# Optimization experiments

Measured on AMD Instinct MI355X. Metric: run time of the kernel, lower is better.

The kernel has to match this reference:

```python
import jax, jax.numpy as jnp
import numpy as np

B, T, D = 1, 4096, 2048
H, G, K = 16, 4, 128   # query heads, kv heads, head_dim
R = H // G             # n_rep = 4
EPS = 1e-6
SCALE = K ** -0.5


def rms_norm(x, scale):
    var = jnp.mean(x.astype(jnp.float32) ** 2, axis=-1, keepdims=True)
    normed = x * jax.lax.rsqrt(var + EPS)
    return (scale * normed).astype(x.dtype)


def apply_rope(x_BTHK, sin_BTK, cos_BTK):
    half = x_BTHK.shape[-1] // 2
    x1, x2 = x_BTHK[..., :half], x_BTHK[..., half:]
    s = sin_BTK[:, :, None, :]
    c = cos_BTK[:, :, None, :]
    return jnp.concatenate([x1 * c - x2 * s, x2 * c + x1 * s], axis=-1).astype(x_BTHK.dtype)


def setup_inputs() -> dict:
    key = jax.random.key(0)
    ks = jax.random.split(key, 8)
    hidden = jax.random.normal(ks[0], (B, T, D), dtype=jnp.float32)
    # rope angles
    inv_freq = 1.0 / (10000.0 ** (jnp.arange(0, K, 2, dtype=jnp.float32) / K))  # [K/2]
    pos = jnp.arange(T, dtype=jnp.float32)
    ang = pos[:, None] * inv_freq[None, :]          # [T, K/2]
    sin = jnp.broadcast_to(jnp.sin(ang)[None], (B, T, K // 2))
    cos = jnp.broadcast_to(jnp.cos(ang)[None], (B, T, K // 2))
    mask = jnp.broadcast_to(jnp.tril(jnp.ones((T, T), dtype=bool))[None], (B, T, T))
    std = D ** -0.5
    Wq = jax.random.normal(ks[1], (D, H * K), dtype=jnp.float32) * std
    Wk = jax.random.normal(ks[2], (D, G * K), dtype=jnp.float32) * std
    Wv = jax.random.normal(ks[3], (D, G * K), dtype=jnp.float32) * std
    Wo = jax.random.normal(ks[4], (H * K, D), dtype=jnp.float32) * ((H * K) ** -0.5)
    q_scale = jnp.ones((K,), dtype=jnp.float32)
    k_scale = jnp.ones((K,), dtype=jnp.float32)
    return {"hidden_BTD": hidden, "sin_BTK": sin, "cos_BTK": cos, "mask": mask,
            "Wq": Wq, "Wk": Wk, "Wv": Wv, "Wo": Wo,
            "q_scale": q_scale, "k_scale": k_scale}


def reference(hidden_BTD, sin_BTK, cos_BTK, mask, Wq, Wk, Wv, Wo, q_scale, k_scale):
    q = rms_norm((hidden_BTD @ Wq).reshape(B, T, H, K), q_scale)
    k = rms_norm((hidden_BTD @ Wk).reshape(B, T, G, K), k_scale)
    v = (hidden_BTD @ Wv).reshape(B, T, G, K)
    q = apply_rope(q, sin_BTK, cos_BTK)
    k = apply_rope(k, sin_BTK, cos_BTK)
    q_BTGRK = q.reshape(B, T, G, R, K)
    logits = jnp.einsum('BTGRK,BSGK->BTSGR', q_BTGRK, k) * SCALE
    neg = float(jnp.finfo(logits.dtype).min)
    logits = jnp.where(mask[:, :, :, None, None], logits, neg)
    weights = jax.nn.softmax(logits.astype(jnp.float32), axis=2).astype(logits.dtype)
    attn = jnp.einsum('BTSGR,BSGK->BTGRK', weights, v)
    return attn.reshape(B, T, H * K) @ Wo
```

## Files before the change

### kernel.cpp

```cpp
#include <hip/hip_runtime.h>
#include <hip/hip_bf16.h>
#include <stdint.h>

#define T_SEQ 4096
#define KVB 64
#define BM 128
#define BN 128
#define BK 64
#define SCL2 (0.08838834764831845f * 1.44269504088896340f)

typedef unsigned short u16;
typedef __attribute__((ext_vector_type(8))) short s16x8;
typedef __attribute__((ext_vector_type(4))) short s16x4;
typedef __attribute__((ext_vector_type(4))) float f32x4;

__device__ __forceinline__ u16 f2bf(float f) {
  union { float f; unsigned u; } a; a.f = f;
  unsigned r = a.u + 0x7fffu + ((a.u >> 16) & 1u);
  return (u16)(r >> 16);
}
__device__ __forceinline__ float bf2f(u16 b) {
  union { unsigned u; float f; } a; a.u = ((unsigned)b) << 16;
  return a.f;
}
__device__ __forceinline__ unsigned cvtpk(float lo, float hi) {
  unsigned r;
  asm volatile("v_cvt_pk_bf16_f32 %0, %1, %2" : "=v"(r) : "v"(lo), "v"(hi));
  return r;
}

__device__ __forceinline__ void gl_lds16(const void* g, void* l) {
  __builtin_amdgcn_global_load_lds((const __attribute__((address_space(1))) void*)g,
                                   (__attribute__((address_space(3))) void*)l, 16, 0, 0);
}

__global__ __launch_bounds__(256) void k_cvt(const float* __restrict__ in, u16* __restrict__ out) {
  int i = (blockIdx.x * 256 + threadIdx.x) * 8;
  const float4* p = (const float4*)(in + i);
  float4 a = p[0], b = p[1];
  s16x8 o;
  o[0] = (short)f2bf(a.x); o[1] = (short)f2bf(a.y); o[2] = (short)f2bf(a.z); o[3] = (short)f2bf(a.w);
  o[4] = (short)f2bf(b.x); o[5] = (short)f2bf(b.y); o[6] = (short)f2bf(b.z); o[7] = (short)f2bf(b.w);
  *(s16x8*)(out + i) = o;
}

__global__ __launch_bounds__(256) void k_transpose_cvt(const float* __restrict__ in, u16* __restrict__ out,
                                                       int R, int C) {
  __shared__ float tile[32][33];
  int c0 = blockIdx.x * 32, r0 = blockIdx.y * 32;
  int tx = threadIdx.x & 31, ty = threadIdx.x >> 5;
#pragma unroll
  for (int k = 0; k < 4; k++) tile[ty + 8 * k][tx] = in[(size_t)(r0 + ty + 8 * k) * C + c0 + tx];
  __syncthreads();
#pragma unroll
  for (int k = 0; k < 4; k++) out[(size_t)(c0 + ty + 8 * k) * R + r0 + tx] = f2bf(tile[tx][ty + 8 * k]);
}

__global__ __launch_bounds__(256, 2) void k_gemm(const u16* __restrict__ A, const u16* __restrict__ Bt,
                                                 u16* __restrict__ Cq, u16* __restrict__ Ck, u16* __restrict__ Cvt,
                                                 float* __restrict__ Cf, int M, int N, int Kd, int mode) {
  __shared__ u16 SM[BM * BK + BN * BK];
  u16* As = SM;
  u16* Bs = SM + BM * BK;
  int tid = threadIdx.x, lane = tid & 63, w = tid >> 6;
  int g = lane >> 4, r16 = lane & 15;
  int m0 = blockIdx.y * BM, n0 = blockIdx.x * BN;
  int wr = w >> 1, wc = w & 1;
  f32x4 acc[4][4] = {};

  for (int kt = 0; kt < Kd; kt += BK) {
#pragma unroll
    for (int i = 0; i < 4; i++) {
      int idx = i * 256 + tid;
      int row = idx >> 3, c = idx & 7;
      int cs = c ^ (row & 7);
      gl_lds16(A + (size_t)(m0 + row) * Kd + kt + cs * 8, As + (i * 256 + w * 64) * 8);
    }
#pragma unroll
    for (int i = 0; i < 4; i++) {
      int idx = i * 256 + tid;
      int row = idx >> 3, c = idx & 7;
      int cs = c ^ (row & 7);
      gl_lds16(Bt + (size_t)(n0 + row) * Kd + kt + cs * 8, Bs + (i * 256 + w * 64) * 8);
    }
    __syncthreads();
#pragma unroll
    for (int kk = 0; kk < 2; kk++) {
      s16x8 af[4], bfr[4];
#pragma unroll
      for (int mi = 0; mi < 4; mi++) {
        int row = wr * 64 + mi * 16 + r16;
        af[mi] = *(const s16x8*)(As + row * 64 + (((kk * 4 + g) ^ (row & 7)) * 8));
      }
#pragma unroll
      for (int ni = 0; ni < 4; ni++) {
        int row = wc * 64 + ni * 16 + r16;
        bfr[ni] = *(const s16x8*)(Bs + row * 64 + (((kk * 4 + g) ^ (row & 7)) * 8));
      }
#pragma unroll
      for (int mi = 0; mi < 4; mi++)
#pragma unroll
        for (int ni = 0; ni < 4; ni++)
          acc[mi][ni] = __builtin_amdgcn_mfma_f32_16x16x32_bf16(af[mi], bfr[ni], acc[mi][ni], 0, 0, 0);
    }
    __syncthreads();
  }

#pragma unroll
  for (int mi = 0; mi < 4; mi++) {
    int rowb = m0 + wr * 64 + mi * 16 + g * 4;
#pragma unroll
    for (int ni = 0; ni < 4; ni++) {
      int ncol0 = n0 + wc * 64 + ni * 16;
      int col = ncol0 + r16;
      if (mode == 0) {
        if (ncol0 < 2048) {
#pragma unroll
          for (int j = 0; j < 4; j++) Cq[(size_t)(rowb + j) * 2048 + col] = f2bf(acc[mi][ni][j]);
        } else if (ncol0 < 2560) {
#pragma unroll
          for (int j = 0; j < 4; j++) Ck[(size_t)(rowb + j) * 512 + (col - 2048)] = f2bf(acc[mi][ni][j]);
        } else {
          s16x4 pk;
#pragma unroll
          for (int j = 0; j < 4; j++) pk[j] = (short)f2bf(acc[mi][ni][j]);
          *(s16x4*)(Cvt + (size_t)(col - 2560) * T_SEQ + rowb) = pk;
        }
      } else {
#pragma unroll
        for (int j = 0; j < 4; j++) Cf[(size_t)(rowb + j) * N + col] = acc[mi][ni][j];
      }
    }
  }
}

__global__ __launch_bounds__(256) void k_normrope(u16* __restrict__ Q, u16* __restrict__ Kc,
                                                  const float* __restrict__ sinT, const float* __restrict__ cosT,
                                                  const float* __restrict__ qsc, const float* __restrict__ ksc) {
  int t = blockIdx.x;
  int w = threadIdx.x >> 6, lane = threadIdx.x & 63;
  int unit = blockIdx.y * 4 + w;
  u16* base;
  const float* sc;
  float fold;
  if (unit < 16) { base = Q + (size_t)t * 2048 + unit * 128; sc = qsc; fold = SCL2; }
  else { base = Kc + (size_t)t * 512 + (unit - 16) * 128; sc = ksc; fold = 1.0f; }
  float x1 = bf2f(base[lane]), x2 = bf2f(base[lane + 64]);
  float ss = x1 * x1 + x2 * x2;
#pragma unroll
  for (int off = 32; off >= 1; off >>= 1) ss += __shfl_xor(ss, off);
  float rinv = rsqrtf(ss * (1.0f / 128.0f) + 1e-6f);
  float n1 = x1 * rinv * sc[lane], n2 = x2 * rinv * sc[lane + 64];
  float s = sinT[t * 64 + lane], c = cosT[t * 64 + lane];
  base[lane] = f2bf((n1 * c - n2 * s) * fold);
  base[lane + 64] = f2bf((n2 * c + n1 * s) * fold);
}

__global__ __launch_bounds__(256, 2) void k_attn(const u16* __restrict__ Q, const u16* __restrict__ Kc,
                                                 const u16* __restrict__ Vt, u16* __restrict__ O) {
  __shared__ u16 SM[36864];
  int tid = threadIdx.x, lane = tid & 63, w = tid >> 6;
  int g = lane >> 4, r16 = lane & 15;

  int bid = blockIdx.x;
  int xcd = bid & 7;
  int k = bid >> 3;
  int slot = k >> 5;
  int c = k & 31;
  int h = xcd * 2 + (c & 1);
  int qb = slot ? (31 - (c >> 1)) : (c >> 1);
  int gh = h >> 2;
  int q0 = qb * 128, qw = q0 + w * 32;
  int nt = 2 * qb + 2;

  s16x8 qf[2][4];
#pragma unroll
  for (int qc = 0; qc < 2; qc++)
#pragma unroll
    for (int dc = 0; dc < 4; dc++)
      qf[qc][dc] = *(const s16x8*)(Q + (size_t)(qw + qc * 16 + r16) * 2048 + h * 128 + dc * 32 + g * 8);

  auto STAGE = [&](int bb, int tt) {
    int kv0 = tt * KVB;
    u16* Kb = SM + bb * 8192;
    u16* Vb = SM + 16384 + bb * 8192;
#pragma unroll
    for (int i = 0; i < 4; i++) {
      int idx = i * 256 + tid;
      int row = idx >> 4, cc = idx & 15;
      int cs = cc ^ (row & 7);
      gl_lds16(Kc + (size_t)(kv0 + row) * 512 + gh * 128 + cs * 8, Kb + (i * 256 + w * 64) * 8);
    }
#pragma unroll
    for (int i = 0; i < 4; i++) {
      int idx = i * 256 + tid;
      int row = idx >> 3, cc = idx & 7;
      int cs = cc ^ (row & 7);
      gl_lds16(Vt + (size_t)(gh * 128 + row) * T_SEQ + kv0 + cs * 8, Vb + (i * 256 + w * 64) * 8);
    }
  };

  f32x4 acc[2][8] = {};
  float mrun[2] = {-3.0e38f, -3.0e38f};
  float lrun[2] = {0.0f, 0.0f};

  STAGE(0, 0);
  __syncthreads();

  for (int t = 0; t < nt; ++t) {
    int kv0 = t * KVB;
    int bb = t & 1;
    STAGE(bb ^ 1, (t + 1 < nt) ? t + 1 : 0);

    if (kv0 <= qw + 31) {
      u16* Kb = SM + bb * 8192;
      u16* Vb = SM + 16384 + bb * 8192;
      u16* Pw = SM + 32768 + w * 1024;

      f32x4 sv[2][4] = {};
      __builtin_amdgcn_s_setprio(1);
#pragma unroll
      for (int kc = 0; kc < 4; kc++) {
        int krow = kc * 16 + r16;
#pragma unroll
        for (int dc = 0; dc < 4; dc++) {
          s16x8 kf = *(const s16x8*)(Kb + krow * 128 + (((dc * 4 + g) ^ (krow & 7)) * 8));
          sv[0][kc] = __builtin_amdgcn_mfma_f32_16x16x32_bf16(kf, qf[0][dc], sv[0][kc], 0, 0, 0);
          sv[1][kc] = __builtin_amdgcn_mfma_f32_16x16x32_bf16(kf, qf[1][dc], sv[1][kc], 0, 0, 0);
        }
      }
      __builtin_amdgcn_s_setprio(0);

#pragma unroll
      for (int qc = 0; qc < 2; qc++) {
        int qg = qw + qc * 16 + r16;
        bool needmask = (kv0 + KVB - 1) > (qw + qc * 16);
        if (needmask) {
#pragma unroll
          for (int kc = 0; kc < 4; kc++)
#pragma unroll
            for (int j2 = 0; j2 < 4; j2++)
              if (kv0 + kc * 16 + g * 4 + j2 > qg) sv[qc][kc][j2] = -3.0e38f;
        }
        float mt = sv[qc][0][0];
#pragma unroll
        for (int kc = 0; kc < 4; kc++)
#pragma unroll
          for (int j2 = 0; j2 < 4; j2++) mt = fmaxf(mt, sv[qc][kc][j2]);
        mt = fmaxf(mt, __shfl_xor(mt, 16));
        mt = fmaxf(mt, __shfl_xor(mt, 32));
        if (__any(mt > mrun[qc] + 8.0f)) {
          float mnew = fmaxf(mrun[qc], mt);
          float al = exp2f(mrun[qc] - mnew);
          mrun[qc] = mnew;
          lrun[qc] *= al;
#pragma unroll
          for (int df = 0; df < 8; df++) acc[qc][df] = acc[qc][df] * al;
        }
        float rs = 0.0f;
#pragma unroll
        for (int kc = 0; kc < 4; kc++) {
          float p0 = exp2f(sv[qc][kc][0] - mrun[qc]);
          float p1 = exp2f(sv[qc][kc][1] - mrun[qc]);
          float p2 = exp2f(sv[qc][kc][2] - mrun[qc]);
          float p3 = exp2f(sv[qc][kc][3] - mrun[qc]);
          rs += (p0 + p1) + (p2 + p3);
          uint2 pk;
          pk.x = cvtpk(p0, p1);
          pk.y = cvtpk(p2, p3);
          int pslot = (kc * 2 + (g >> 1)) ^ (r16 & 7);
          *(uint2*)((char*)Pw + r16 * 128 + pslot * 16 + (g & 1) * 8) = pk;
        }
        rs += __shfl_xor(rs, 16);
        rs += __shfl_xor(rs, 32);
        lrun[qc] += rs;

        __builtin_amdgcn_s_setprio(1);
#pragma unroll
        for (int st = 0; st < 2; st++) {
          s16x8 pf = *(const s16x8*)((char*)Pw + r16 * 128 + (((st * 4 + g) ^ (r16 & 7)) * 16));
#pragma unroll
          for (int df = 0; df < 8; df++) {
            int vrow = df * 16 + r16;
            s16x8 vf = *(const s16x8*)(Vb + vrow * 64 + (((st * 4 + g) ^ (vrow & 7)) * 8));
            acc[qc][df] = __builtin_amdgcn_mfma_f32_16x16x32_bf16(vf, pf, acc[qc][df], 0, 0, 0);
          }
        }
        __builtin_amdgcn_s_setprio(0);
      }
    }
    __syncthreads();
  }

  char* ob = (char*)SM + w * 8192;
#pragma unroll
  for (int qc = 0; qc < 2; qc++) {
    float linv = 1.0f / lrun[qc];
#pragma unroll
    for (int df = 0; df < 8; df++) {
      s16x4 pk;
#pragma unroll
      for (int j2 = 0; j2 < 4; j2++) pk[j2] = (short)f2bf(acc[qc][df][j2] * linv);
      int row = qc * 16 + r16;
      int c16 = df * 2 + (g >> 1);
      *(s16x4*)(ob + row * 256 + ((c16 ^ (row & 7)) << 4) + (g & 1) * 8) = pk;
    }
  }
#pragma unroll
  for (int i = 0; i < 8; i++) {
    int idx = i * 64 + lane;
    int row = idx >> 4, cc = idx & 15;
    s16x8 v = *(const s16x8*)(ob + row * 256 + ((cc ^ (row & 7)) << 4));
    *(s16x8*)(O + (size_t)(qw + row) * 2048 + h * 128 + cc * 8) = v;
  }
}

extern "C" void kernel_launch(void* const* d_in, const int* in_sizes, int n_in,
                              void* d_out, int out_size, void* d_ws, size_t ws_size,
                              hipStream_t stream) {
  const float* hidden = (const float*)d_in[0];
  const float* sinT = (const float*)d_in[1];
  const float* cosT = (const float*)d_in[2];
  const float* Wq = (const float*)d_in[4];
  const float* Wk = (const float*)d_in[5];
  const float* Wv = (const float*)d_in[6];
  const float* Wo = (const float*)d_in[7];
  const float* qsc = (const float*)d_in[8];
  const float* ksc = (const float*)d_in[9];
  float* out = (float*)d_out;

  char* ws = (char*)d_ws;
  u16* Xb   = (u16*)(ws + 0);
  u16* Bqkv = (u16*)(ws + 16777216);
  u16* Wot  = (u16*)(ws + 29360128);
  u16* Qraw = (u16*)(ws + 37748736);
  u16* Kraw = (u16*)(ws + 54525952);
  u16* Vt   = (u16*)(ws + 58720256);
  u16* Oat  = (u16*)(ws + 62914560);

  k_cvt<<<dim3(4096), dim3(256), 0, stream>>>(hidden, Xb);
  k_transpose_cvt<<<dim3(64, 64), dim3(256), 0, stream>>>(Wq, Bqkv, 2048, 2048);
  k_transpose_cvt<<<dim3(16, 64), dim3(256), 0, stream>>>(Wk, Bqkv + 2048 * 2048, 2048, 512);
  k_transpose_cvt<<<dim3(16, 64), dim3(256), 0, stream>>>(Wv, Bqkv + 2560 * 2048, 2048, 512);
  k_transpose_cvt<<<dim3(64, 64), dim3(256), 0, stream>>>(Wo, Wot, 2048, 2048);

  k_gemm<<<dim3(24, 32), dim3(256), 0, stream>>>(Xb, Bqkv, Qraw, Kraw, Vt, (float*)nullptr,
                                                 4096, 3072, 2048, 0);
  k_normrope<<<dim3(4096, 5), dim3(256), 0, stream>>>(Qraw, Kraw, sinT, cosT, qsc, ksc);
  k_attn<<<dim3(512), dim3(256), 0, stream>>>(Qraw, Kraw, Vt, Oat);
  k_gemm<<<dim3(16, 32), dim3(256), 0, stream>>>(Oat, Wot, (u16*)nullptr, (u16*)nullptr, (u16*)nullptr,
                                                 out, 4096, 2048, 2048, 1);
}
```

Measured before the change: 274.4 us.

## Split attention KV tiles across wave pairs with smaller query blocks and LDS merge

The attention kernel now uses 64-row query blocks, 1024 blocks in total, ordered longest-first. The four waves form two query halves by two KV halves, so each wave handles 32 queries against 32 of the 64 staged KV rows. The partial softmax states (max, sum, accumulator) of the two KV-split waves are merged through LDS at the end before the bf16 write. This aims to raise parallelism and improve causal load balance, at the cost of more LDS (72KB, which may limit occupancy) and an extra reduction pass.

```diff
diff --git a/kernel.cpp b/kernel.cpp
--- a/kernel.cpp
+++ b/kernel.cpp
@@ -158,32 +158,32 @@
 
 __global__ __launch_bounds__(256, 2) void k_attn(const u16* __restrict__ Q, const u16* __restrict__ Kc,
                                                  const u16* __restrict__ Vt, u16* __restrict__ O) {
-  __shared__ u16 SM[36864];
+  __shared__ __align__(16) char SMc[73728];
   int tid = threadIdx.x, lane = tid & 63, w = tid >> 6;
   int g = lane >> 4, r16 = lane & 15;
+  int qs = w >> 1, ks = w & 1;
 
   int bid = blockIdx.x;
   int xcd = bid & 7;
-  int k = bid >> 3;
-  int slot = k >> 5;
-  int c = k & 31;
-  int h = xcd * 2 + (c & 1);
-  int qb = slot ? (31 - (c >> 1)) : (c >> 1);
+  int lid = bid >> 3;
+  int h = xcd * 2 + (lid & 1);
+  int qb = 63 - (lid >> 1);
   int gh = h >> 2;
-  int q0 = qb * 128, qw = q0 + w * 32;
-  int nt = 2 * qb + 2;
+  int q0 = qb * 64;
+  int qwv = q0 + qs * 32;
+  int nt = qb + 1;
 
   s16x8 qf[2][4];
 #pragma unroll
   for (int qc = 0; qc < 2; qc++)
 #pragma unroll
     for (int dc = 0; dc < 4; dc++)
-      qf[qc][dc] = *(const s16x8*)(Q + (size_t)(qw + qc * 16 + r16) * 2048 + h * 128 + dc * 32 + g * 8);
+      qf[qc][dc] = *(const s16x8*)(Q + (size_t)(qwv + qc * 16 + r16) * 2048 + h * 128 + dc * 32 + g * 8);
 
   auto STAGE = [&](int bb, int tt) {
     int kv0 = tt * KVB;
-    u16* Kb = SM + bb * 8192;
-    u16* Vb = SM + 16384 + bb * 8192;
+    u16* Kb = (u16*)(SMc + bb * 16384);
+    u16* Vb = (u16*)(SMc + 32768 + bb * 16384);
 #pragma unroll
     for (int i = 0; i < 4; i++) {
       int idx = i * 256 + tid;
@@ -212,19 +212,20 @@
     int bb = t & 1;
     STAGE(bb ^ 1, (t + 1 < nt) ? t + 1 : 0);
 
-    if (kv0 <= qw + 31) {
-      u16* Kb = SM + bb * 8192;
-      u16* Vb = SM + 16384 + bb * 8192;
-      u16* Pw = SM + 32768 + w * 1024;
-
-      f32x4 sv[2][4] = {};
+    int kvw = kv0 + ks * 32;
+    if (kvw <= qwv + 31) {
+      u16* Kb = (u16*)(SMc + bb * 16384);
+      u16* Vb = (u16*)(SMc + 32768 + bb * 16384);
+      char* Pwb = SMc + 65536 + w * 2048;
+
+      f32x4 sv[2][2] = {};
       __builtin_amdgcn_s_setprio(1);
 #pragma unroll
-      for (int kc = 0; kc < 4; kc++) {
-        int krow = kc * 16 + r16;
+      for (int kc = 0; kc < 2; kc++) {
+        int krow = ks * 32 + kc * 16 + r16;
 #pragma unroll
         for (int dc = 0; dc < 4; dc++) {
-          s16x8 kf = *(const s16x8*)(Kb + krow * 128 + (((dc * 4 + g) ^ (krow & 7)) * 8));
+          s16x8 kf = *(const s16x8*)((u16*)Kb + krow * 128 + (((dc * 4 + g) ^ (krow & 7)) * 8));
           sv[0][kc] = __builtin_amdgcn_mfma_f32_16x16x32_bf16(kf, qf[0][dc], sv[0][kc], 0, 0, 0);
           sv[1][kc] = __builtin_amdgcn_mfma_f32_16x16x32_bf16(kf, qf[1][dc], sv[1][kc], 0, 0, 0);
         }
@@ -233,18 +234,18 @@
 
 #pragma unroll
       for (int qc = 0; qc < 2; qc++) {
-        int qg = qw + qc * 16 + r16;
-        bool needmask = (kv0 + KVB - 1) > (qw + qc * 16);
+        int qg = qwv + qc * 16 + r16;
+        bool needmask = (kvw + 31) > (qwv + qc * 16);
         if (needmask) {
 #pragma unroll
-          for (int kc = 0; kc < 4; kc++)
+          for (int kc = 0; kc < 2; kc++)
 #pragma unroll
             for (int j2 = 0; j2 < 4; j2++)
-              if (kv0 + kc * 16 + g * 4 + j2 > qg) sv[qc][kc][j2] = -3.0e38f;
+              if (kvw + kc * 16 + g * 4 + j2 > qg) sv[qc][kc][j2] = -3.0e38f;
         }
         float mt = sv[qc][0][0];
 #pragma unroll
-        for (int kc = 0; kc < 4; kc++)
+        for (int kc = 0; kc < 2; kc++)
 #pragma unroll
           for (int j2 = 0; j2 < 4; j2++) mt = fmaxf(mt, sv[qc][kc][j2]);
         mt = fmaxf(mt, __shfl_xor(mt, 16));
@@ -259,7 +260,7 @@
         }
         float rs = 0.0f;
 #pragma unroll
-        for (int kc = 0; kc < 4; kc++) {
+        for (int kc = 0; kc < 2; kc++) {
           float p0 = exp2f(sv[qc][kc][0] - mrun[qc]);
           float p1 = exp2f(sv[qc][kc][1] - mrun[qc]);
           float p2 = exp2f(sv[qc][kc][2] - mrun[qc]);
@@ -268,50 +269,75 @@
           uint2 pk;
           pk.x = cvtpk(p0, p1);
           pk.y = cvtpk(p2, p3);
-          int pslot = (kc * 2 + (g >> 1)) ^ (r16 & 7);
-          *(uint2*)((char*)Pw + r16 * 128 + pslot * 16 + (g & 1) * 8) = pk;
+          int unit = ((qc << 2) | (kc << 1) | (g >> 1)) ^ (r16 & 7);
+          *(uint2*)(Pwb + r16 * 128 + unit * 16 + (g & 1) * 8) = pk;
         }
         rs += __shfl_xor(rs, 16);
         rs += __shfl_xor(rs, 32);
         lrun[qc] += rs;
-
-        __builtin_amdgcn_s_setprio(1);
-#pragma unroll
-        for (int st = 0; st < 2; st++) {
-          s16x8 pf = *(const s16x8*)((char*)Pw + r16 * 128 + (((st * 4 + g) ^ (r16 & 7)) * 16));
-#pragma unroll
-          for (int df = 0; df < 8; df++) {
-            int vrow = df * 16 + r16;
-            s16x8 vf = *(const s16x8*)(Vb + vrow * 64 + (((st * 4 + g) ^ (vrow & 7)) * 8));
-            acc[qc][df] = __builtin_amdgcn_mfma_f32_16x16x32_bf16(vf, pf, acc[qc][df], 0, 0, 0);
-          }
-        }
-        __builtin_amdgcn_s_setprio(0);
-      }
+      }
+
+      __builtin_amdgcn_s_setprio(1);
+      s16x8 pf0 = *(const s16x8*)(Pwb + r16 * 128 + (((0 * 4 + g) ^ (r16 & 7)) * 16));
+      s16x8 pf1 = *(const s16x8*)(Pwb + r16 * 128 + (((1 * 4 + g) ^ (r16 & 7)) * 16));
+#pragma unroll
+      for (int df = 0; df < 8; df++) {
+        int vrow = df * 16 + r16;
+        s16x8 vf = *(const s16x8*)((u16*)Vb + vrow * 64 + (((ks * 4 + g) ^ (vrow & 7)) * 8));
+        acc[0][df] = __builtin_amdgcn_mfma_f32_16x16x32_bf16(vf, pf0, acc[0][df], 0, 0, 0);
+        acc[1][df] = __builtin_amdgcn_mfma_f32_16x16x32_bf16(vf, pf1, acc[1][df], 0, 0, 0);
+      }
+      __builtin_amdgcn_s_setprio(0);
     }
     __syncthreads();
   }
 
-  char* ob = (char*)SM + w * 8192;
+  float* ml = (float*)(SMc + 65536);
+  if (g < 2) {
+    float mv = g ? mrun[1] : mrun[0];
+    float lv = g ? lrun[1] : lrun[0];
+    int mi = ((w * 2 + g) * 16 + r16) * 2;
+    ml[mi] = mv;
+    ml[mi + 1] = lv;
+  }
+  __syncthreads();
+  int pw = w ^ 1;
+  float scale[2];
 #pragma unroll
   for (int qc = 0; qc < 2; qc++) {
-    float linv = 1.0f / lrun[qc];
+    float pm = ml[((pw * 2 + qc) * 16 + r16) * 2];
+    float pl = ml[((pw * 2 + qc) * 16 + r16) * 2 + 1];
+    float ms = fmaxf(mrun[qc], pm);
+    float aS = exp2f(mrun[qc] - ms);
+    float aP = exp2f(pm - ms);
+    float ls = lrun[qc] * aS + pl * aP;
+    scale[qc] = aS / ls;
+  }
+  char* obw = SMc + qs * 16384 + ks * 32768;
+#pragma unroll
+  for (int qc = 0; qc < 2; qc++)
 #pragma unroll
     for (int df = 0; df < 8; df++) {
-      s16x4 pk;
-#pragma unroll
-      for (int j2 = 0; j2 < 4; j2++) pk[j2] = (short)f2bf(acc[qc][df][j2] * linv);
-      int row = qc * 16 + r16;
-      int c16 = df * 2 + (g >> 1);
-      *(s16x4*)(ob + row * 256 + ((c16 ^ (row & 7)) << 4) + (g & 1) * 8) = pk;
-    }
-  }
-#pragma unroll
-  for (int i = 0; i < 8; i++) {
-    int idx = i * 64 + lane;
-    int row = idx >> 4, cc = idx & 15;
-    s16x8 v = *(const s16x8*)(ob + row * 256 + ((cc ^ (row & 7)) << 4));
-    *(s16x8*)(O + (size_t)(qw + row) * 2048 + h * 128 + cc * 8) = v;
+      f32x4 v = acc[qc][df] * scale[qc];
+      int r = qc * 16 + r16;
+      int u = df * 4 + g;
+      int up = u ^ ((r & 7) << 2);
+      *(f32x4*)(obw + r * 512 + up * 16) = v;
+    }
+  __syncthreads();
+#pragma unroll
+  for (int it = 0; it < 8; it++) {
+    int item = it * 256 + tid;
+    int qs2 = item >> 10, rem = item & 1023;
+    int r = rem >> 5, u = rem & 31;
+    int up = u ^ ((r & 7) << 2);
+    f32x4 a = *(const f32x4*)(SMc + qs2 * 16384 + r * 512 + up * 16);
+    f32x4 b = *(const f32x4*)(SMc + 32768 + qs2 * 16384 + r * 512 + up * 16);
+    f32x4 sSum = a + b;
+    uint2 pk;
+    pk.x = cvtpk(sSum[0], sSum[1]);
+    pk.y = cvtpk(sSum[2], sSum[3]);
+    *(uint2*)(O + (size_t)(q0 + qs2 * 32 + r) * 2048 + h * 128 + u * 4) = pk;
   }
 }
 
@@ -347,7 +373,7 @@
   k_gemm<<<dim3(24, 32), dim3(256), 0, stream>>>(Xb, Bqkv, Qraw, Kraw, Vt, (float*)nullptr,
                                                  4096, 3072, 2048, 0);
   k_normrope<<<dim3(4096, 5), dim3(256), 0, stream>>>(Qraw, Kraw, sinT, cosT, qsc, ksc);
-  k_attn<<<dim3(512), dim3(256), 0, stream>>>(Qraw, Kraw, Vt, Oat);
+  k_attn<<<dim3(1024), dim3(256), 0, stream>>>(Qraw, Kraw, Vt, Oat);
   k_gemm<<<dim3(16, 32), dim3(256), 0, stream>>>(Oat, Wot, (u16*)nullptr, (u16*)nullptr, (u16*)nullptr,
                                                  out, 4096, 2048, 2048, 1);
 }
```

Measured after the change: 268.3 us. 1.02x faster.
